# Kernel tuning notes

Hardware: AMD Instinct MI355X
Metric: run time of the kernel (lower is better)

Reference implementation:

```python
import jax, jax.numpy as jnp
import numpy as np

B, L, C = 32, 8192, 64
LEVELS = 3  # detail kernels 3,5,9 with pads 1,2,4


def _conv1d(x, w, b, pad):
    # x: [B, C, L], w: [O, I, K] (torch Conv1d layout), b: [O]
    y = jax.lax.conv_general_dilated(
        x, w, window_strides=(1,), padding=[(pad, pad)],
        dimension_numbers=('NCH', 'OIH', 'NCH'))
    return y + b[None, :, None]


def _block(xc, w1, b1, w2, b2, pad):
    # Conv1d(k) -> ReLU -> Conv1d(k=1)
    h = jax.nn.relu(_conv1d(xc, w1, b1, pad))
    return _conv1d(h, w2, b2, 0)


def setup_inputs() -> dict:
    key = jax.random.key(0)
    ks = jax.random.split(key, 20)
    s = 0.05  # keep activations stable
    inp = {
        'x': jax.random.normal(ks[0], (B, L, C), jnp.float32),
        'rec_weights': jnp.ones((LEVELS + 1,), jnp.float32) / (LEVELS + 1),
        'trend_w1': jax.random.normal(ks[1], (C, C, 3), jnp.float32) * s,
        'trend_b1': jnp.zeros((C,), jnp.float32),
        'trend_w2': jax.random.normal(ks[2], (C, C, 1), jnp.float32) * s,
        'trend_b2': jnp.zeros((C,), jnp.float32),
    }
    kernels = [3, 5, 9]
    for i, k in enumerate(kernels, start=1):
        inp[f'd{i}_w1'] = jax.random.normal(ks[2 + 2 * i], (C, C, k), jnp.float32) * s
        inp[f'd{i}_b1'] = jnp.zeros((C,), jnp.float32)
        inp[f'd{i}_w2'] = jax.random.normal(ks[3 + 2 * i], (C, C, 1), jnp.float32) * s
        inp[f'd{i}_b2'] = jnp.zeros((C,), jnp.float32)
    return inp


def reference(x, rec_weights,
              trend_w1, trend_b1, trend_w2, trend_b2,
              d1_w1, d1_b1, d1_w2, d1_b2,
              d2_w1, d2_b1, d2_w2, d2_b2,
              d3_w1, d3_b1, d3_w2, d3_b2):
    # component_fusion forward: x [B, L, C] -> [B, L, C]
    xc = jnp.transpose(x, (0, 2, 1))  # [B, C, L]
    trend = _block(xc, trend_w1, trend_b1, trend_w2, trend_b2, 1)
    d1 = _block(xc, d1_w1, d1_b1, d1_w2, d1_b2, 1)   # k=3, pad=1
    d2 = _block(xc, d2_w1, d2_b1, d2_w2, d2_b2, 2)   # k=5, pad=2
    d3 = _block(xc, d3_w1, d3_b1, d3_w2, d3_b2, 4)   # k=9, pad=4
    w = jax.nn.softmax(rec_weights)
    fused = w[0] * trend + w[1] * d1 + w[2] * d2 + w[3] * d3
    return jnp.transpose(fused, (0, 2, 1))
```

## Files before the change

### kernel.cpp

```cpp
#include <hip/hip_runtime.h>


constexpr int Bn = 32, Ln = 8192;
constexpr int NT = 256;
constexpr int HALO = 4;
constexpr int XROWS = NT + 2 * HALO;
constexpr int RS = 72;
constexpr int NSLICE = 24;

constexpr int BRS[NSLICE] = {0,0,0,0, 1,1,1,1, 2,2,2,2,2,2, 3,3,3,3,3,3,3,3,3,3};
constexpr int DKS[NSLICE] = {0,1,2,-1, 0,1,2,-1, 0,1,2,3,4,-1, 0,1,2,3,4,5,6,7,8,-1};
constexpr int PPB[4] = {1, 1, 2, 4};

using bf16x8 = __attribute__((ext_vector_type(8))) __bf16;
using f32x4  = __attribute__((ext_vector_type(4))) float;
using u16x8  = __attribute__((ext_vector_type(8))) unsigned short;
using u16x4  = __attribute__((ext_vector_type(4))) unsigned short;
using s16x4  = __attribute__((ext_vector_type(4))) short;

struct Ptrs {
    const float* x;
    const float* rw;
    const float* w1[4];
    const float* b1[4];
    const float* w2[4];
    const float* b2[4];
};

__device__ __forceinline__ unsigned short f2bf(float f) {
    __bf16 h = (__bf16)f;
    return __builtin_bit_cast(unsigned short, h);
}

#if defined(__has_builtin)
#  if __has_builtin(__builtin_amdgcn_mfma_f32_16x16x16bf16_1k)
#    define HAVE_MFMA16 1
#  endif
#endif

__device__ __forceinline__ void mfma16(f32x4& c, u16x4 a, u16x4 b) {
#ifdef HAVE_MFMA16
    c = __builtin_amdgcn_mfma_f32_16x16x16bf16_1k(
            __builtin_bit_cast(s16x4, a), __builtin_bit_cast(s16x4, b), c, 0, 0, 0);
#else
    asm("v_mfma_f32_16x16x16_bf16 %0, %1, %2, %0" : "+v"(c) : "v"(a), "v"(b));
#endif
}

__global__ void prep_kernel(Ptrs p, unsigned short* __restrict__ frag, float* __restrict__ hdr) {
    int tid = threadIdx.x;
    float v0 = p.rw[0], v1 = p.rw[1], v2 = p.rw[2], v3 = p.rw[3];
    float m = fmaxf(fmaxf(v0, v1), fmaxf(v2, v3));
    float e0 = expf(v0 - m), e1 = expf(v1 - m), e2 = expf(v2 - m), e3 = expf(v3 - m);
    float s = e0 + e1 + e2 + e3;
    float w[4] = {e0 / s, e1 / s, e2 / s, e3 / s};

    if (blockIdx.x == 0) {
        if (tid < 4) hdr[tid] = w[tid];
        if (tid < 64) {
            float fb = 0.f;
            #pragma unroll
            for (int i = 0; i < 4; i++) fb += w[i] * p.b2[i][tid];
            hdr[4 + tid] = fb;
        }
    }

    const int kk[4] = {3, 3, 5, 9};
    const int sbase[4] = {0, 4, 8, 14};

    for (int idx = blockIdx.x * blockDim.x + tid; idx < NSLICE * 4096; idx += gridDim.x * blockDim.x) {
        int sl = idx >> 12;
        int e = idx & 4095;
        int br = 3;
        #pragma unroll
        for (int i = 2; i >= 0; i--) if (sl < sbase[i + 1]) br = i;
        int local = sl - sbase[br];
        unsigned short val;
        if (local < kk[br]) {
            int blk = e >> 9;
            int ks = blk >> 2, mt = blk & 3;
            int sub = e & 511;
            int lane = sub >> 3, j = sub & 7;
            int co = mt * 16 + (lane & 15);
            int ci = ks * 32 + (lane >> 4) * 8 + j;
            val = f2bf(p.w1[br][(co * 64 + ci) * kk[br] + local]);
        } else {
            int c = e >> 9;
            int sub = e & 511;
            int lane = sub >> 3;
            int rest = sub & 7;
            int h = rest >> 2, j = rest & 3;
            int f = c * 2 + h;
            int kb = f >> 2, mt = f & 3;
            int co = mt * 16 + (lane & 15);
            int ci = kb * 16 + (lane >> 4) * 4 + j;
            val = f2bf(w[br] * p.w2[br][co * 64 + ci]);
        }
        frag[idx] = val;
    }
}

template <int S>
__device__ __forceinline__ void period(const unsigned short* __restrict__ frag,
                                       const unsigned short* xs,
                                       const float* b1l,
                                       int lane, int wl0,
                                       f32x4 (&acc)[4][4], f32x4 (&fused)[4][4],
                                       bf16x8 (&cur)[8], bf16x8 (&nxt)[8]) {
    if constexpr (S + 1 < NSLICE) {
        const unsigned short* nb = frag + (size_t)(S + 1) * 4096 + lane * 8;
        #pragma unroll
        for (int c = 0; c < 8; c++)
            nxt[c] = __builtin_bit_cast(bf16x8, *(const u16x8*)(nb + c * 512));
    }

    constexpr int br = BRS[S];
    constexpr int dk = DKS[S];
    int col = lane & 15, kg = lane >> 4;

    if constexpr (dk >= 0) {
        if constexpr (dk == 0) {
            #pragma unroll
            for (int mt = 0; mt < 4; mt++)
                #pragma unroll
                for (int nt = 0; nt < 4; nt++)
                    acc[mt][nt] = f32x4{0.f, 0.f, 0.f, 0.f};
        }
        constexpr int PP = PPB[br];
        #pragma unroll
        for (int ks = 0; ks < 2; ks++) {
            bf16x8 bfr[4];
            #pragma unroll
            for (int nt = 0; nt < 4; nt++) {
                int row = wl0 + nt * 16 + col + (HALO - PP) + dk;
                bfr[nt] = __builtin_bit_cast(bf16x8, *(const u16x8*)&xs[row * RS + ks * 32 + kg * 8]);
            }
            __builtin_amdgcn_s_setprio(1);
            #pragma unroll
            for (int mt = 0; mt < 4; mt++)
                #pragma unroll
                for (int nt = 0; nt < 4; nt++)
                    acc[mt][nt] = __builtin_amdgcn_mfma_f32_16x16x32_bf16(cur[ks * 4 + mt], bfr[nt], acc[mt][nt], 0, 0, 0);
            __builtin_amdgcn_s_setprio(0);
        }
    } else {
        const float* bb = b1l + br * 64;
        f32x4 bv[4];
        #pragma unroll
        for (int mt = 0; mt < 4; mt++) bv[mt] = *(const f32x4*)&bb[mt * 16 + kg * 4];
        #pragma unroll
        for (int kb = 0; kb < 4; kb++) {
            u16x4 hb[4];
            #pragma unroll
            for (int nt = 0; nt < 4; nt++) {
                u16x4 h;
                #pragma unroll
                for (int r = 0; r < 4; r++) h[r] = f2bf(fmaxf(acc[kb][nt][r] + bv[kb][r], 0.f));
                hb[nt] = h;
            }
            __builtin_amdgcn_s_setprio(1);
            #pragma unroll
            for (int mt2 = 0; mt2 < 4; mt2++) {
                int f = kb * 4 + mt2;
                u16x8 u = __builtin_bit_cast(u16x8, cur[f >> 1]);
                int h4 = (f & 1) * 4;
                u16x4 afr = {u[h4], u[h4 + 1], u[h4 + 2], u[h4 + 3]};
                #pragma unroll
                for (int nt = 0; nt < 4; nt++)
                    mfma16(fused[mt2][nt], afr, hb[nt]);
            }
            __builtin_amdgcn_s_setprio(0);
        }
    }
}

template <int S>
__device__ __forceinline__ void chain(const unsigned short* __restrict__ frag,
                                      const unsigned short* xs,
                                      const float* b1l, int lane, int wl0,
                                      f32x4 (&acc)[4][4], f32x4 (&fused)[4][4],
                                      bf16x8 (&A)[8], bf16x8 (&B)[8]) {
    if constexpr (S & 1) period<S>(frag, xs, b1l, lane, wl0, acc, fused, B, A);
    else                 period<S>(frag, xs, b1l, lane, wl0, acc, fused, A, B);
    if constexpr (S + 1 < NSLICE)
        chain<S + 1>(frag, xs, b1l, lane, wl0, acc, fused, A, B);
}

__global__ __launch_bounds__(256, 2) void wavelet_main(Ptrs p,
                                                       const unsigned short* __restrict__ frag,
                                                       const float* __restrict__ hdr,
                                                       float* __restrict__ out) {
    __shared__ unsigned short xs[XROWS * RS];
    __shared__ float b1l[4 * 64];
    __shared__ float fbl[64];

    int tid = threadIdx.x;
    int b = blockIdx.x >> 5;
    int t0 = (blockIdx.x & 31) * NT;

    {
        int c0 = (tid & 7) * 8;
        int rbase = tid >> 3;
        #pragma unroll
        for (int it = 0; it < 9; it++) {
            int rr = it * 32 + rbase;
            if (rr < XROWS) {
                int l = t0 + rr - HALO;
                u16x8 v = {0, 0, 0, 0, 0, 0, 0, 0};
                if (l >= 0 && l < Ln) {
                    const float* src = &p.x[((size_t)b * Ln + l) * 64 + c0];
                    f32x4 a0 = *(const f32x4*)src;
                    f32x4 a1 = *(const f32x4*)(src + 4);
                    #pragma unroll
                    for (int r = 0; r < 4; r++) { v[r] = f2bf(a0[r]); v[4 + r] = f2bf(a1[r]); }
                }
                *(u16x8*)&xs[rr * RS + c0] = v;
            }
        }
    }
    b1l[tid] = p.b1[tid >> 6][tid & 63];
    if (tid < 64) fbl[tid] = hdr[4 + tid];

    int lane = tid & 63;
    int wl0 = (tid >> 6) * 64;
    int kg = lane >> 4;

    bf16x8 A[8], B[8];
    {
        const unsigned short* b0 = frag + lane * 8;
        #pragma unroll
        for (int c = 0; c < 8; c++)
            A[c] = __builtin_bit_cast(bf16x8, *(const u16x8*)(b0 + c * 512));
    }

    f32x4 acc[4][4];
    f32x4 fused[4][4];
    #pragma unroll
    for (int mt = 0; mt < 4; mt++)
        #pragma unroll
        for (int nt = 0; nt < 4; nt++)
            fused[mt][nt] = f32x4{0.f, 0.f, 0.f, 0.f};

    __syncthreads();

    chain<0>(frag, xs, b1l, lane, wl0, acc, fused, A, B);

#ifndef HAVE_MFMA16
    asm volatile("s_nop 7\ns_nop 7");
#endif

    int col = lane & 15;
    f32x4 fb[4];
    #pragma unroll
    for (int mt = 0; mt < 4; mt++) fb[mt] = *(const f32x4*)&fbl[mt * 16 + kg * 4];
    #pragma unroll
    for (int nt = 0; nt < 4; nt++) {
        int l = t0 + wl0 + nt * 16 + col;
        #pragma unroll
        for (int mt = 0; mt < 4; mt++) {
            f32x4 v;
            #pragma unroll
            for (int r = 0; r < 4; r++) v[r] = fused[mt][nt][r] + fb[mt][r];
            *(f32x4*)&out[((size_t)b * Ln + l) * 64 + mt * 16 + kg * 4] = v;
        }
    }
}

extern "C" void kernel_launch(void* const* d_in, const int* in_sizes, int n_in,
                              void* d_out, int out_size, void* d_ws, size_t ws_size,
                              hipStream_t stream) {
    Ptrs p;
    p.x  = (const float*)d_in[0];
    p.rw = (const float*)d_in[1];
    for (int i = 0; i < 4; i++) {
        p.w1[i] = (const float*)d_in[2 + 4 * i];
        p.b1[i] = (const float*)d_in[3 + 4 * i];
        p.w2[i] = (const float*)d_in[4 + 4 * i];
        p.b2[i] = (const float*)d_in[5 + 4 * i];
    }
    float* hdr = (float*)d_ws;
    unsigned short* frag = (unsigned short*)((char*)d_ws + 512);

    hipLaunchKernelGGL(prep_kernel, dim3(96), dim3(256), 0, stream, p, frag, hdr);
    hipLaunchKernelGGL(wavelet_main, dim3(Bn * (Ln / NT)), dim3(256), 0, stream, p, frag, hdr,
                       (float*)d_out);
}
```

Before: 61.75 us.

## Halve per-wave tile and split weight prefetch to cut registers, raise occupancy

Each block now covers 128 time steps instead of 256, so every wave handles 32 columns and keeps half as many accumulators. The double-buffered weight fragments (two arrays of eight) become two half-slice buffers of four, and the next slice's first half is loaded mid-period. Launch bounds go from 2 to 3 blocks per SM to use the freed registers. The cost is twice as many blocks, a larger halo share, and each weight fragment loaded from global or L2 being reused across half as many columns.

```diff
diff --git a/kernel.cpp b/kernel.cpp
--- a/kernel.cpp
+++ b/kernel.cpp
@@ -2,7 +2,7 @@
 
 
 constexpr int Bn = 32, Ln = 8192;
-constexpr int NT = 256;
+constexpr int NT = 128;
 constexpr int HALO = 4;
 constexpr int XROWS = NT + 2 * HALO;
 constexpr int RS = 72;
@@ -105,42 +105,62 @@
                                        const unsigned short* xs,
                                        const float* b1l,
                                        int lane, int wl0,
-                                       f32x4 (&acc)[4][4], f32x4 (&fused)[4][4],
-                                       bf16x8 (&cur)[8], bf16x8 (&nxt)[8]) {
-    if constexpr (S + 1 < NSLICE) {
-        const unsigned short* nb = frag + (size_t)(S + 1) * 4096 + lane * 8;
-        #pragma unroll
-        for (int c = 0; c < 8; c++)
-            nxt[c] = __builtin_bit_cast(bf16x8, *(const u16x8*)(nb + c * 512));
-    }
-
+                                       f32x4 (&acc)[4][2], f32x4 (&fused)[4][2],
+                                       bf16x8 (&W0)[4], bf16x8 (&W1)[4]) {
     constexpr int br = BRS[S];
     constexpr int dk = DKS[S];
     int col = lane & 15, kg = lane >> 4;
 
+    {
+        const unsigned short* bc = frag + (size_t)S * 4096 + lane * 8;
+        #pragma unroll
+        for (int c = 0; c < 4; c++)
+            W1[c] = __builtin_bit_cast(bf16x8, *(const u16x8*)(bc + (size_t)(4 + c) * 512));
+    }
+
     if constexpr (dk >= 0) {
         if constexpr (dk == 0) {
             #pragma unroll
             for (int mt = 0; mt < 4; mt++)
                 #pragma unroll
-                for (int nt = 0; nt < 4; nt++)
+                for (int nt = 0; nt < 2; nt++)
                     acc[mt][nt] = f32x4{0.f, 0.f, 0.f, 0.f};
         }
         constexpr int PP = PPB[br];
-        #pragma unroll
-        for (int ks = 0; ks < 2; ks++) {
-            bf16x8 bfr[4];
-            #pragma unroll
-            for (int nt = 0; nt < 4; nt++) {
+        {
+            bf16x8 bfr[2];
+            #pragma unroll
+            for (int nt = 0; nt < 2; nt++) {
                 int row = wl0 + nt * 16 + col + (HALO - PP) + dk;
-                bfr[nt] = __builtin_bit_cast(bf16x8, *(const u16x8*)&xs[row * RS + ks * 32 + kg * 8]);
+                bfr[nt] = __builtin_bit_cast(bf16x8, *(const u16x8*)&xs[row * RS + kg * 8]);
             }
             __builtin_amdgcn_s_setprio(1);
             #pragma unroll
             for (int mt = 0; mt < 4; mt++)
                 #pragma unroll
-                for (int nt = 0; nt < 4; nt++)
-                    acc[mt][nt] = __builtin_amdgcn_mfma_f32_16x16x32_bf16(cur[ks * 4 + mt], bfr[nt], acc[mt][nt], 0, 0, 0);
+                for (int nt = 0; nt < 2; nt++)
+                    acc[mt][nt] = __builtin_amdgcn_mfma_f32_16x16x32_bf16(W0[mt], bfr[nt], acc[mt][nt], 0, 0, 0);
+            __builtin_amdgcn_s_setprio(0);
+        }
+        if constexpr (S + 1 < NSLICE) {
+            const unsigned short* bn = frag + (size_t)(S + 1) * 4096 + lane * 8;
+            #pragma unroll
+            for (int c = 0; c < 4; c++)
+                W0[c] = __builtin_bit_cast(bf16x8, *(const u16x8*)(bn + (size_t)c * 512));
+        }
+        {
+            bf16x8 bfr[2];
+            #pragma unroll
+            for (int nt = 0; nt < 2; nt++) {
+                int row = wl0 + nt * 16 + col + (HALO - PP) + dk;
+                bfr[nt] = __builtin_bit_cast(bf16x8, *(const u16x8*)&xs[row * RS + 32 + kg * 8]);
+            }
+            __builtin_amdgcn_s_setprio(1);
+            #pragma unroll
+            for (int mt = 0; mt < 4; mt++)
+                #pragma unroll
+                for (int nt = 0; nt < 2; nt++)
+                    acc[mt][nt] = __builtin_amdgcn_mfma_f32_16x16x32_bf16(W1[mt], bfr[nt], acc[mt][nt], 0, 0, 0);
             __builtin_amdgcn_s_setprio(0);
         }
     } else {
@@ -149,10 +169,10 @@
         #pragma unroll
         for (int mt = 0; mt < 4; mt++) bv[mt] = *(const f32x4*)&bb[mt * 16 + kg * 4];
         #pragma unroll
-        for (int kb = 0; kb < 4; kb++) {
-            u16x4 hb[4];
-            #pragma unroll
-            for (int nt = 0; nt < 4; nt++) {
+        for (int kb = 0; kb < 2; kb++) {
+            u16x4 hb[2];
+            #pragma unroll
+            for (int nt = 0; nt < 2; nt++) {
                 u16x4 h;
                 #pragma unroll
                 for (int r = 0; r < 4; r++) h[r] = f2bf(fmaxf(acc[kb][nt][r] + bv[kb][r], 0.f));
@@ -162,11 +182,40 @@
             #pragma unroll
             for (int mt2 = 0; mt2 < 4; mt2++) {
                 int f = kb * 4 + mt2;
-                u16x8 u = __builtin_bit_cast(u16x8, cur[f >> 1]);
+                u16x8 u = __builtin_bit_cast(u16x8, W0[f >> 1]);
                 int h4 = (f & 1) * 4;
                 u16x4 afr = {u[h4], u[h4 + 1], u[h4 + 2], u[h4 + 3]};
                 #pragma unroll
-                for (int nt = 0; nt < 4; nt++)
+                for (int nt = 0; nt < 2; nt++)
+                    mfma16(fused[mt2][nt], afr, hb[nt]);
+            }
+            __builtin_amdgcn_s_setprio(0);
+        }
+        if constexpr (S + 1 < NSLICE) {
+            const unsigned short* bn = frag + (size_t)(S + 1) * 4096 + lane * 8;
+            #pragma unroll
+            for (int c = 0; c < 4; c++)
+                W0[c] = __builtin_bit_cast(bf16x8, *(const u16x8*)(bn + (size_t)c * 512));
+        }
+        #pragma unroll
+        for (int kb = 2; kb < 4; kb++) {
+            u16x4 hb[2];
+            #pragma unroll
+            for (int nt = 0; nt < 2; nt++) {
+                u16x4 h;
+                #pragma unroll
+                for (int r = 0; r < 4; r++) h[r] = f2bf(fmaxf(acc[kb][nt][r] + bv[kb][r], 0.f));
+                hb[nt] = h;
+            }
+            __builtin_amdgcn_s_setprio(1);
+            #pragma unroll
+            for (int mt2 = 0; mt2 < 4; mt2++) {
+                int f = kb * 4 + mt2;
+                u16x8 u = __builtin_bit_cast(u16x8, W1[(f >> 1) - 4]);
+                int h4 = (f & 1) * 4;
+                u16x4 afr = {u[h4], u[h4 + 1], u[h4 + 2], u[h4 + 3]};
+                #pragma unroll
+                for (int nt = 0; nt < 2; nt++)
                     mfma16(fused[mt2][nt], afr, hb[nt]);
             }
             __builtin_amdgcn_s_setprio(0);
@@ -178,15 +227,14 @@
 __device__ __forceinline__ void chain(const unsigned short* __restrict__ frag,
                                       const unsigned short* xs,
                                       const float* b1l, int lane, int wl0,
-                                      f32x4 (&acc)[4][4], f32x4 (&fused)[4][4],
-                                      bf16x8 (&A)[8], bf16x8 (&B)[8]) {
-    if constexpr (S & 1) period<S>(frag, xs, b1l, lane, wl0, acc, fused, B, A);
-    else                 period<S>(frag, xs, b1l, lane, wl0, acc, fused, A, B);
+                                      f32x4 (&acc)[4][2], f32x4 (&fused)[4][2],
+                                      bf16x8 (&W0)[4], bf16x8 (&W1)[4]) {
+    period<S>(frag, xs, b1l, lane, wl0, acc, fused, W0, W1);
     if constexpr (S + 1 < NSLICE)
-        chain<S + 1>(frag, xs, b1l, lane, wl0, acc, fused, A, B);
-}
-
-__global__ __launch_bounds__(256, 2) void wavelet_main(Ptrs p,
+        chain<S + 1>(frag, xs, b1l, lane, wl0, acc, fused, W0, W1);
+}
+
+__global__ __launch_bounds__(256, 3) void wavelet_main(Ptrs p,
                                                        const unsigned short* __restrict__ frag,
                                                        const float* __restrict__ hdr,
                                                        float* __restrict__ out) {
@@ -195,14 +243,14 @@
     __shared__ float fbl[64];
 
     int tid = threadIdx.x;
-    int b = blockIdx.x >> 5;
-    int t0 = (blockIdx.x & 31) * NT;
+    int b = blockIdx.x >> 6;
+    int t0 = (blockIdx.x & 63) * NT;
 
     {
         int c0 = (tid & 7) * 8;
         int rbase = tid >> 3;
         #pragma unroll
-        for (int it = 0; it < 9; it++) {
+        for (int it = 0; it < 5; it++) {
             int rr = it * 32 + rbase;
             if (rr < XROWS) {
                 int l = t0 + rr - HALO;
@@ -222,28 +270,28 @@
     if (tid < 64) fbl[tid] = hdr[4 + tid];
 
     int lane = tid & 63;
-    int wl0 = (tid >> 6) * 64;
+    int wl0 = (tid >> 6) * 32;
     int kg = lane >> 4;
 
-    bf16x8 A[8], B[8];
+    bf16x8 W0[4], W1[4];
     {
         const unsigned short* b0 = frag + lane * 8;
         #pragma unroll
-        for (int c = 0; c < 8; c++)
-            A[c] = __builtin_bit_cast(bf16x8, *(const u16x8*)(b0 + c * 512));
-    }
-
-    f32x4 acc[4][4];
-    f32x4 fused[4][4];
+        for (int c = 0; c < 4; c++)
+            W0[c] = __builtin_bit_cast(bf16x8, *(const u16x8*)(b0 + (size_t)c * 512));
+    }
+
+    f32x4 acc[4][2];
+    f32x4 fused[4][2];
     #pragma unroll
     for (int mt = 0; mt < 4; mt++)
         #pragma unroll
-        for (int nt = 0; nt < 4; nt++)
+        for (int nt = 0; nt < 2; nt++)
             fused[mt][nt] = f32x4{0.f, 0.f, 0.f, 0.f};
 
     __syncthreads();
 
-    chain<0>(frag, xs, b1l, lane, wl0, acc, fused, A, B);
+    chain<0>(frag, xs, b1l, lane, wl0, acc, fused, W0, W1);
 
 #ifndef HAVE_MFMA16
     asm volatile("s_nop 7\ns_nop 7");
@@ -254,7 +302,7 @@
     #pragma unroll
     for (int mt = 0; mt < 4; mt++) fb[mt] = *(const f32x4*)&fbl[mt * 16 + kg * 4];
     #pragma unroll
-    for (int nt = 0; nt < 4; nt++) {
+    for (int nt = 0; nt < 2; nt++) {
         int l = t0 + wl0 + nt * 16 + col;
         #pragma unroll
         for (int mt = 0; mt < 4; mt++) {
```

Result: slower. 72.14 us (+16.8%).
